# Kernel tuning notes

Hardware: AMD Instinct MI355X
Metric: run time of the kernel (lower is better)

The kernel has to match this reference:

```python
import jax, jax.numpy as jnp
import numpy as np

B, S, D, H = 2, 2048, 1024, 16
HD = D // H  # 64


def setup_inputs() -> dict:
    key = jax.random.key(0)
    ks = jax.random.split(key, 7)
    scale = 1.0 / np.sqrt(D)
    return {
        "embeddings": jax.random.normal(ks[0], (B, S, D), dtype=jnp.float32),
        "W_kv": jax.random.uniform(ks[1], (D, 2 * D), jnp.float32, -scale, scale),
        "b_kv": jax.random.uniform(ks[2], (2 * D,), jnp.float32, -scale, scale),
        "W_q": jax.random.uniform(ks[3], (D, D), jnp.float32, -scale, scale),
        "b_q": jax.random.uniform(ks[4], (D,), jnp.float32, -scale, scale),
        "W_o": jax.random.uniform(ks[5], (D, D), jnp.float32, -scale, scale),
        "b_o": jax.random.uniform(ks[6], (D,), jnp.float32, -scale, scale),
    }


def reference(embeddings, W_kv, b_kv, W_q, b_q, W_o, b_o):
    # kv projection -> [B, S, H, 2*HD] -> [B, H, S, 2*HD]
    kv = (embeddings @ W_kv + b_kv).reshape(B, S, H, 2 * HD).transpose(0, 2, 1, 3)
    q = (embeddings @ W_q + b_q).reshape(B, S, H, HD).transpose(0, 2, 1, 3)
    k, v = kv[..., :HD], kv[..., HD:]
    # naive scaled dot-product attention (full [B,H,S,S] score matrix)
    scores = jnp.einsum("bhqd,bhkd->bhqk", q, k) / jnp.sqrt(jnp.float32(HD))
    attn = jax.nn.softmax(scores, axis=-1)
    ctx = jnp.einsum("bhqk,bhkd->bhqd", attn, v)  # [B,H,S,HD]
    ctx = ctx.transpose(0, 2, 1, 3).reshape(B, S, D)
    return ctx @ W_o + b_o
```

## Files before the change

### kernel.cpp

```cpp
#include <hip/hip_runtime.h>
#include <hip/hip_bf16.h>


typedef unsigned short ushort;
typedef __attribute__((ext_vector_type(4))) float f32x4;
typedef __attribute__((ext_vector_type(16))) float f32x16;
typedef __attribute__((ext_vector_type(8))) __bf16 bf16x8;
typedef __attribute__((ext_vector_type(8))) unsigned short u16x8;
typedef __attribute__((ext_vector_type(4))) unsigned short u16x4;
typedef __attribute__((ext_vector_type(4))) unsigned int u32x4;

#define LOG2E 1.44269504088896340736f

constexpr int Bc = 2, Sc = 2048, Dc = 1024, Hc = 16, HDc = 64;

__device__ inline ushort f2bf(float f) {
    unsigned u = __builtin_bit_cast(unsigned, f);
    u += 0x7fffu + ((u >> 16) & 1u);
    return (ushort)(u >> 16);
}

__device__ inline float fexp2(float x) {
#if __has_builtin(__builtin_amdgcn_exp2f)
    return __builtin_amdgcn_exp2f(x);
#else
    return exp2f(x);
#endif
}

__device__ inline void gload16(const void* g, void* l) {
    __builtin_amdgcn_global_load_lds((const __attribute__((address_space(1))) void*)g,
                                     (__attribute__((address_space(3))) void*)l, 16, 0, 0);
}

__device__ inline f32x4 mfma16(bf16x8 a, bf16x8 b, f32x4 c) {
    return __builtin_amdgcn_mfma_f32_16x16x32_bf16(a, b, c, 0, 0, 0);
}
__device__ inline f32x16 mfma32(bf16x8 a, bf16x8 b, f32x16 c) {
    return __builtin_amdgcn_mfma_f32_32x32x16_bf16(a, b, c, 0, 0, 0);
}
__device__ inline unsigned cvtpk(float lo, float hi_) {
    unsigned r; asm("v_cvt_pk_bf16_f32 %0, %1, %2" : "=v"(r) : "v"(lo), "v"(hi_)); return r;
}
__device__ inline void swap32(unsigned& a, unsigned& b) {
    asm("v_permlane32_swap_b32 %0, %1" : "+v"(a), "+v"(b));
}

__global__ __launch_bounds__(256) void prep_k(const float* __restrict__ emb,
                                              ushort* __restrict__ embb,
                                              const float* __restrict__ Wkv,
                                              const float* __restrict__ Wq,
                                              const float* __restrict__ Wo,
                                              ushort* __restrict__ WtAll) {
    const int bid = blockIdx.x;
    if (bid < 2048) {
        int i = bid * 256 + threadIdx.x;
        const float4* p = (const float4*)emb;
        float4 a = p[2 * i], b = p[2 * i + 1];
        u16x8 r;
        r[0] = f2bf(a.x); r[1] = f2bf(a.y); r[2] = f2bf(a.z); r[3] = f2bf(a.w);
        r[4] = f2bf(b.x); r[5] = f2bf(b.y); r[6] = f2bf(b.z); r[7] = f2bf(b.w);
        ((u16x8*)embb)[i] = r;
        return;
    }
    __shared__ float t[32][33];
    int tb = bid - 2048;
    const float* W; int N, rowofs;
    if (tb < 2048)      { W = Wkv; N = 2048; rowofs = 0; }
    else if (tb < 3072) { W = Wq;  N = 1024; rowofs = 2048; tb -= 2048; }
    else                { W = Wo;  N = 1024; rowofs = 3072; tb -= 3072; }
    const int nbx = N >> 5;
    const int bx = tb % nbx, by = tb / nbx;
    const int tx = threadIdx.x & 31, ty = threadIdx.x >> 5;
    const int bj = bx * 32, bi = by * 32;
#pragma unroll
    for (int i = 0; i < 4; i++) {
        int r = ty + i * 8;
        t[r][tx] = W[(size_t)(bi + r) * N + bj + tx];
    }
    __syncthreads();
#pragma unroll
    for (int i = 0; i < 4; i++) {
        int r = ty + i * 8;
        WtAll[(size_t)(rowofs + bj + r) * 1024 + bi + tx] = f2bf(t[tx][r]);
    }
}

template <int MODE>
__global__ __launch_bounds__(256) void gemm_bt_k(const ushort* __restrict__ A,
                                                 const ushort* __restrict__ Bt,
                                                 const float* __restrict__ bias,
                                                 const float* __restrict__ bias2,
                                                 void* __restrict__ Cout,
                                                 ushort* __restrict__ Vout,
                                                 ushort* __restrict__ Qout,
                                                 int M, int N, int K) {
    __shared__ __align__(16) char sA[2][8192];
    __shared__ __align__(16) char sB[2][8192];
    const int tid = threadIdx.x;
    const int nbc = N >> 7;
    const int cpx = (gridDim.x >> 3);
    const int swzb = (blockIdx.x & 7) * cpx + (blockIdx.x >> 3);
    const int brow = swzb / nbc, bcol = swzb % nbc;
    const int w = tid >> 6, lane = tid & 63;
    const int wr = w >> 1, wc = w & 1;
    const int lg = lane >> 4, l16 = lane & 15;

    f32x4 acc[4][4] = {};

    const int r0 = tid >> 2;
    const int sl = (tid & 3) ^ (r0 & 3);
    const ushort* a0 = A + (size_t)(brow * 128 + r0) * K + sl * 8;
    const ushort* a1 = A + (size_t)(brow * 128 + 64 + r0) * K + sl * 8;
    const ushort* b0 = Bt + (size_t)(bcol * 128 + r0) * K + sl * 8;
    const ushort* b1 = Bt + (size_t)(bcol * 128 + 64 + r0) * K + sl * 8;

    const int arow = wr * 64 + l16;
    const int bcolr = wc * 64 + l16;

    auto STAGE = [&](int buf, int k0) {
        gload16(a0 + k0, sA[buf] + w * 1024);
        gload16(a1 + k0, sA[buf] + 4096 + w * 1024);
        gload16(b0 + k0, sB[buf] + w * 1024);
        gload16(b1 + k0, sB[buf] + 4096 + w * 1024);
    };

    const int nk = K >> 5;
    STAGE(0, 0);

    for (int k0 = 0; k0 < nk; k0++) {
        const int buf = k0 & 1;
        if (k0 < nk - 1) {
            STAGE(buf ^ 1, (k0 + 1) << 5);
            asm volatile("s_waitcnt vmcnt(4)" ::: "memory");
        } else {
            asm volatile("s_waitcnt vmcnt(0)" ::: "memory");
        }
        __builtin_amdgcn_s_barrier();
        __builtin_amdgcn_sched_barrier(0);

        bf16x8 af[4], bfr[4];
#pragma unroll
        for (int rf = 0; rf < 4; rf++) {
            int rr = arow + rf * 16;
            af[rf] = *(const bf16x8*)(sA[buf] + rr * 64 + ((lg * 16) ^ ((rr & 3) << 4)));
        }
#pragma unroll
        for (int cf = 0; cf < 4; cf++) {
            int rr = bcolr + cf * 16;
            bfr[cf] = *(const bf16x8*)(sB[buf] + rr * 64 + ((lg * 16) ^ ((rr & 3) << 4)));
        }
#pragma unroll
        for (int rf = 0; rf < 4; rf++)
#pragma unroll
            for (int cf = 0; cf < 4; cf++)
                acc[rf][cf] = mfma16(af[rf], bfr[cf], acc[rf][cf]);
        __builtin_amdgcn_s_barrier();
    }

#pragma unroll
    for (int cf = 0; cf < 4; cf++) {
        const int col = bcol * 128 + wc * 64 + cf * 16 + l16;
        if constexpr (MODE == 3) {
            if (col < 2048) {
                const float bv = bias[col];
                const int h = col >> 7, lo = col & 127;
#pragma unroll
                for (int rf = 0; rf < 4; rf++) {
                    int row = brow * 128 + wr * 64 + rf * 16 + lg * 4;
                    int b = row >> 11, s = row & 2047;
                    if (lo < 64) {
                        ushort* Kout = (ushort*)Cout;
#pragma unroll
                        for (int r = 0; r < 4; r++)
                            Kout[((size_t)(b * 16 + h) * 2048 + s + r) * 64 + lo] =
                                f2bf(acc[rf][cf][r] + bv);
                    } else {
                        u16x4 pk;
#pragma unroll
                        for (int r = 0; r < 4; r++) pk[r] = f2bf(acc[rf][cf][r] + bv);
                        *(u16x4*)(Vout + ((size_t)(b * 16 + h) * 64 + (lo - 64)) * 2048 + s) = pk;
                    }
                }
            } else {
                const int qc = col - 2048;
                const float bv = bias2[qc];
                const float qs = 0.125f * LOG2E;
#pragma unroll
                for (int rf = 0; rf < 4; rf++) {
                    int row = brow * 128 + wr * 64 + rf * 16 + lg * 4;
#pragma unroll
                    for (int r = 0; r < 4; r++)
                        Qout[(size_t)(row + r) * 1024 + qc] =
                            f2bf((acc[rf][cf][r] + bv) * qs);
                }
            }
        } else {
            const float bv = bias[col];
#pragma unroll
            for (int rf = 0; rf < 4; rf++) {
                int row = brow * 128 + wr * 64 + rf * 16 + lg * 4;
#pragma unroll
                for (int r = 0; r < 4; r++) {
                    float v = acc[rf][cf][r] + bv;
                    if (MODE == 1) ((float*)Cout)[(size_t)(row + r) * N + col] = v;
                    else           ((ushort*)Cout)[(size_t)(row + r) * N + col] = f2bf(v);
                }
            }
        }
    }
}

__global__ __launch_bounds__(256, 2) void attn2_k(const ushort* __restrict__ Qg,
                                                  const ushort* __restrict__ Kg,
                                                  const ushort* __restrict__ Vg,
                                                  ushort* __restrict__ ctx) {
    __shared__ __align__(16) char sK[2][8192];
    __shared__ __align__(16) char sV[2][8192];
    __shared__ float lx2[256];
    const int tid = threadIdx.x;
    const int wg = ((blockIdx.x & 7) << 6) | (blockIdx.x >> 3);
    const int bh = wg >> 4, qt = wg & 15;
    const int b = bh >> 4, h = bh & 15;
    const int w = tid >> 6, lane = tid & 63;
    const int ql = lane & 31, hi = lane >> 5;
    const int ksub = w & 1;
    const int qq = w >> 1;

    const ushort* Kh = Kg + (size_t)bh * (Sc * 64);
    const ushort* Vh = Vg + (size_t)bh * (64 * Sc);

    const int qrow0 = qt * 128 + qq * 64 + ql;
    bf16x8 qf[2][4];
#pragma unroll
    for (int qg = 0; qg < 2; qg++) {
        const ushort* qp = Qg + ((size_t)(b * Sc + qrow0 + qg * 32)) * Dc + h * HDc + hi * 8;
#pragma unroll
        for (int jd = 0; jd < 4; jd++) qf[qg][jd] = *(const bf16x8*)(qp + jd * 16);
    }

    const u16x8 ones_u = {0x3F80, 0x3F80, 0x3F80, 0x3F80, 0x3F80, 0x3F80, 0x3F80, 0x3F80};
    const bf16x8 ones8 = __builtin_bit_cast(bf16x8, ones_u);

    const int rw = w * 16 + (lane >> 3);
    const int sl = (lane & 7) ^ (lane >> 3);

    f32x16 o[2][2] = {};
    f32x16 ls[2] = {};
    const float MH = 8.0f * LOG2E;
    const int sw = (ql & 7) << 4;

    auto STAGE = [&](int buf, int kt) {
#pragma unroll
        for (int j = 0; j < 2; j++) {
            gload16(Kh + (size_t)(kt * 64 + rw + 8 * j) * 64 + sl * 8,
                    sK[buf] + w * 2048 + j * 1024);
            gload16(Vh + (size_t)(rw + 8 * j) * Sc + kt * 64 + sl * 8,
                    sV[buf] + w * 2048 + j * 1024);
        }
    };

    int cur = 0;
    STAGE(0, 0);

    constexpr int NT = Sc / 64;
    for (int kt = 0; kt < NT; kt++) {
        if (kt < NT - 1) {
            STAGE(cur ^ 1, kt + 1);
            asm volatile("s_waitcnt vmcnt(4)" ::: "memory");
        } else {
            asm volatile("s_waitcnt vmcnt(0)" ::: "memory");
        }
        __builtin_amdgcn_s_barrier();
        __builtin_amdgcn_sched_barrier(0);

        bf16x8 kf[4];
        {
            const char* kb = sK[cur] + (ksub * 32 + ql) * 128;
#pragma unroll
            for (int jd = 0; jd < 4; jd++)
                kf[jd] = *(const bf16x8*)(kb + ((jd * 32 + hi * 16) ^ sw));
        }

        f32x16 st[2];
#pragma unroll
        for (int qg = 0; qg < 2; qg++)
#pragma unroll
            for (int i = 0; i < 16; i++) st[qg][i] = -MH;
        __builtin_amdgcn_s_setprio(1);
#pragma unroll
        for (int qg = 0; qg < 2; qg++)
#pragma unroll
            for (int jd = 0; jd < 4; jd++)
                st[qg] = mfma32(kf[jd], qf[qg][jd], st[qg]);
        __builtin_amdgcn_s_setprio(0);

#pragma unroll
        for (int qg = 0; qg < 2; qg++)
#pragma unroll
            for (int i = 0; i < 16; i++) st[qg][i] = fexp2(st[qg][i]);

        bf16x8 pf[2][2];
#pragma unroll
        for (int qg = 0; qg < 2; qg++) {
            unsigned a0 = cvtpk(st[qg][0],  st[qg][1]);
            unsigned a1 = cvtpk(st[qg][2],  st[qg][3]);
            unsigned a2 = cvtpk(st[qg][4],  st[qg][5]);
            unsigned a3 = cvtpk(st[qg][6],  st[qg][7]);
            swap32(a0, a2); swap32(a1, a3);
            u32x4 f0v = {a0, a1, a2, a3};
            pf[qg][0] = __builtin_bit_cast(bf16x8, f0v);
            unsigned c0 = cvtpk(st[qg][8],  st[qg][9]);
            unsigned c1 = cvtpk(st[qg][10], st[qg][11]);
            unsigned c2 = cvtpk(st[qg][12], st[qg][13]);
            unsigned c3 = cvtpk(st[qg][14], st[qg][15]);
            swap32(c0, c2); swap32(c1, c3);
            u32x4 f1v = {c0, c1, c2, c3};
            pf[qg][1] = __builtin_bit_cast(bf16x8, f1v);
        }

        bf16x8 vf[2][2];
#pragma unroll
        for (int dg = 0; dg < 2; dg++) {
            const char* vb = sV[cur] + (dg * 32 + ql) * 128;
#pragma unroll
            for (int ks = 0; ks < 2; ks++)
                vf[dg][ks] = *(const bf16x8*)(vb + ((ksub * 64 + ks * 32 + hi * 16) ^ sw));
        }

        __builtin_amdgcn_s_setprio(1);
#pragma unroll
        for (int qg = 0; qg < 2; qg++)
#pragma unroll
            for (int ks = 0; ks < 2; ks++) {
                o[0][qg] = mfma32(vf[0][ks], pf[qg][ks], o[0][qg]);
                o[1][qg] = mfma32(vf[1][ks], pf[qg][ks], o[1][qg]);
                ls[qg]   = mfma32(ones8,     pf[qg][ks], ls[qg]);
            }
        __builtin_amdgcn_s_setprio(0);

        __builtin_amdgcn_s_barrier();
        cur ^= 1;
    }

    __syncthreads();
    float* ox = qq ? (float*)sV : (float*)sK;
    if (ksub) {
#pragma unroll
        for (int dg = 0; dg < 2; dg++)
#pragma unroll
            for (int qg = 0; qg < 2; qg++)
#pragma unroll
                for (int i = 0; i < 16; i++)
                    ox[((dg * 2 + qg) * 16 + i) * 64 + lane] = o[dg][qg][i];
        lx2[(qq * 2 + 0) * 64 + lane] = ls[0][0];
        lx2[(qq * 2 + 1) * 64 + lane] = ls[1][0];
    }
    __syncthreads();
    if (!ksub) {
#pragma unroll
        for (int dg = 0; dg < 2; dg++)
#pragma unroll
            for (int qg = 0; qg < 2; qg++)
#pragma unroll
                for (int i = 0; i < 16; i++)
                    o[dg][qg][i] += ox[((dg * 2 + qg) * 16 + i) * 64 + lane];
        const float inv0 = 1.0f / (ls[0][0] + lx2[(qq * 2 + 0) * 64 + lane]);
        const float inv1 = 1.0f / (ls[1][0] + lx2[(qq * 2 + 1) * 64 + lane]);
#pragma unroll
        for (int qg = 0; qg < 2; qg++) {
            const float inv = qg ? inv1 : inv0;
            ushort* cp = ctx + ((size_t)(b * Sc + qrow0 + qg * 32)) * Dc + h * HDc;
#pragma unroll
            for (int dg = 0; dg < 2; dg++)
#pragma unroll
                for (int g = 0; g < 4; g++) {
                    u16x4 pk;
#pragma unroll
                    for (int r = 0; r < 4; r++)
                        pk[r] = f2bf(o[dg][qg][g * 4 + r] * inv);
                    *(u16x4*)(cp + dg * 32 + g * 8 + hi * 4) = pk;
                }
        }
    }
}

extern "C" void kernel_launch(void* const* d_in, const int* in_sizes, int n_in,
                              void* d_out, int out_size, void* d_ws, size_t ws_size,
                              hipStream_t stream) {
    const float* emb  = (const float*)d_in[0];
    const float* W_kv = (const float*)d_in[1];
    const float* b_kv = (const float*)d_in[2];
    const float* W_q  = (const float*)d_in[3];
    const float* b_q  = (const float*)d_in[4];
    const float* W_o  = (const float*)d_in[5];
    const float* b_o  = (const float*)d_in[6];
    float* out = (float*)d_out;

    const int BS = Bc * Sc;
    ushort* embb  = (ushort*)d_ws;
    ushort* wallt = embb  + (size_t)BS * Dc;
    ushort* wot   = wallt + (size_t)3 * Dc * Dc;
    ushort* Kb    = wallt + (size_t)4 * Dc * Dc;
    ushort* Vtb   = Kb    + (size_t)32 * Sc * HDc;
    ushort* Qb    = Vtb   + (size_t)32 * Sc * HDc;
    ushort* ctxb  = Qb    + (size_t)BS * Dc;

    prep_k<<<6144, 256, 0, stream>>>(emb, embb, W_kv, W_q, W_o, wallt);

    gemm_bt_k<3><<<(BS / 128) * (3072 / 128), 256, 0, stream>>>(
        embb, wallt, b_kv, b_q, Kb, Vtb, Qb, BS, 3072, Dc);

    attn2_k<<<Bc * Hc * (Sc / 128), 256, 0, stream>>>(Qb, Kb, Vtb, ctxb);

    gemm_bt_k<1><<<(BS / 128) * (Dc / 128), 256, 0, stream>>>(
        ctxb, wot, b_o, nullptr, out, nullptr, nullptr, BS, Dc, Dc);
}
```

Baseline: 115.0 us.

## Use 256x256-tile 512-thread GEMM kernel for fused QKV projection

Replaces the 128x128-tile QKV projection GEMM with a new 256x256-tile kernel using 8 waves and BK=64 double-buffered LDS staging with an XOR swizzle. Each wave computes 128x64, which raises arithmetic intensity per LDS byte and halves global traffic per FLOP. The grid becomes 16x12=192 blocks, fewer than the CU count on MI355X, so some CUs sit idle. The 128 KB of LDS per block may also limit occupancy. The older MODE 3 epilogue is removed from the generic GEMM.

```diff
diff --git a/kernel.cpp b/kernel.cpp
--- a/kernel.cpp
+++ b/kernel.cpp
@@ -86,14 +86,127 @@
     }
 }
 
+__global__ __launch_bounds__(512, 2) void gemm256_kv_k(const ushort* __restrict__ A,
+                                                       const ushort* __restrict__ Bt,
+                                                       const float* __restrict__ bias,
+                                                       const float* __restrict__ bias2,
+                                                       ushort* __restrict__ Kout,
+                                                       ushort* __restrict__ Vout,
+                                                       ushort* __restrict__ Qout,
+                                                       int N, int K) {
+    __shared__ __align__(16) char sA[2][32768];
+    __shared__ __align__(16) char sB[2][32768];
+    const int tid = threadIdx.x;
+    const int nbc = N >> 8;
+    const int cpx = (gridDim.x >> 3);
+    const int swzb = (blockIdx.x & 7) * cpx + (blockIdx.x >> 3);
+    const int brow = swzb / nbc, bcol = swzb % nbc;
+    const int w = tid >> 6, lane = tid & 63;
+    const int wr = w >> 2, wc = w & 3;
+    const int lg = lane >> 4, l16 = lane & 15;
+
+    f32x4 acc[8][4] = {};
+
+    const int srow = tid >> 3;
+    const int schunk = (tid & 7) ^ (srow & 7);
+    const ushort* aP[4];
+    const ushort* bP[4];
+#pragma unroll
+    for (int s = 0; s < 4; s++) {
+        aP[s] = A  + (size_t)(brow * 256 + s * 64 + srow) * K + schunk * 8;
+        bP[s] = Bt + (size_t)(bcol * 256 + s * 64 + srow) * K + schunk * 8;
+    }
+
+    auto STAGE_ALL = [&](int buf, int k0) {
+#pragma unroll
+        for (int s = 0; s < 4; s++)
+            gload16(aP[s] + k0, sA[buf] + s * 8192 + w * 1024);
+#pragma unroll
+        for (int s = 0; s < 4; s++)
+            gload16(bP[s] + k0, sB[buf] + s * 8192 + w * 1024);
+    };
+
+    const int aro = wr * 128 + l16;
+    const int bro = wc * 64 + l16;
+    const int axor = l16 & 7;
+
+    const int nk = K >> 6;
+    STAGE_ALL(0, 0);
+
+    for (int kt = 0; kt < nk; kt++) {
+        const int buf = kt & 1;
+        if (kt < nk - 1) {
+            STAGE_ALL(buf ^ 1, (kt + 1) << 6);
+            asm volatile("s_waitcnt vmcnt(8)" ::: "memory");
+        } else {
+            asm volatile("s_waitcnt vmcnt(0)" ::: "memory");
+        }
+        __builtin_amdgcn_s_barrier();
+        __builtin_amdgcn_sched_barrier(0);
+
+#pragma unroll
+        for (int ks = 0; ks < 2; ks++) {
+            bf16x8 af[8], bfr[4];
+#pragma unroll
+            for (int rf = 0; rf < 8; rf++)
+                af[rf] = *(const bf16x8*)(sA[buf] + (aro + rf * 16) * 128 +
+                                          ((((ks << 2) | lg) ^ axor) << 4));
+#pragma unroll
+            for (int cf = 0; cf < 4; cf++)
+                bfr[cf] = *(const bf16x8*)(sB[buf] + (bro + cf * 16) * 128 +
+                                           ((((ks << 2) | lg) ^ axor) << 4));
+#pragma unroll
+            for (int rf = 0; rf < 8; rf++)
+#pragma unroll
+                for (int cf = 0; cf < 4; cf++)
+                    acc[rf][cf] = mfma16(af[rf], bfr[cf], acc[rf][cf]);
+        }
+        __builtin_amdgcn_s_barrier();
+    }
+
+#pragma unroll
+    for (int cf = 0; cf < 4; cf++) {
+        const int col = bcol * 256 + wc * 64 + cf * 16 + l16;
+        if (col < 2048) {
+            const float bv = bias[col];
+            const int h = col >> 7, lo = col & 127;
+#pragma unroll
+            for (int rf = 0; rf < 8; rf++) {
+                int row = brow * 256 + wr * 128 + rf * 16 + lg * 4;
+                int b = row >> 11, s = row & 2047;
+                if (lo < 64) {
+#pragma unroll
+                    for (int r = 0; r < 4; r++)
+                        Kout[((size_t)(b * 16 + h) * 2048 + s + r) * 64 + lo] =
+                            f2bf(acc[rf][cf][r] + bv);
+                } else {
+                    u16x4 pk;
+#pragma unroll
+                    for (int r = 0; r < 4; r++) pk[r] = f2bf(acc[rf][cf][r] + bv);
+                    *(u16x4*)(Vout + ((size_t)(b * 16 + h) * 64 + (lo - 64)) * 2048 + s) = pk;
+                }
+            }
+        } else {
+            const int qc = col - 2048;
+            const float bv = bias2[qc];
+            const float qs = 0.125f * LOG2E;
+#pragma unroll
+            for (int rf = 0; rf < 8; rf++) {
+                int row = brow * 256 + wr * 128 + rf * 16 + lg * 4;
+#pragma unroll
+                for (int r = 0; r < 4; r++)
+                    Qout[(size_t)(row + r) * 1024 + qc] =
+                        f2bf((acc[rf][cf][r] + bv) * qs);
+            }
+        }
+    }
+}
+
 template <int MODE>
 __global__ __launch_bounds__(256) void gemm_bt_k(const ushort* __restrict__ A,
                                                  const ushort* __restrict__ Bt,
                                                  const float* __restrict__ bias,
-                                                 const float* __restrict__ bias2,
                                                  void* __restrict__ Cout,
-                                                 ushort* __restrict__ Vout,
-                                                 ushort* __restrict__ Qout,
                                                  int M, int N, int K) {
     __shared__ __align__(16) char sA[2][8192];
     __shared__ __align__(16) char sB[2][8192];
@@ -161,51 +274,15 @@
 #pragma unroll
     for (int cf = 0; cf < 4; cf++) {
         const int col = bcol * 128 + wc * 64 + cf * 16 + l16;
-        if constexpr (MODE == 3) {
-            if (col < 2048) {
-                const float bv = bias[col];
-                const int h = col >> 7, lo = col & 127;
-#pragma unroll
-                for (int rf = 0; rf < 4; rf++) {
-                    int row = brow * 128 + wr * 64 + rf * 16 + lg * 4;
-                    int b = row >> 11, s = row & 2047;
-                    if (lo < 64) {
-                        ushort* Kout = (ushort*)Cout;
-#pragma unroll
-                        for (int r = 0; r < 4; r++)
-                            Kout[((size_t)(b * 16 + h) * 2048 + s + r) * 64 + lo] =
-                                f2bf(acc[rf][cf][r] + bv);
-                    } else {
-                        u16x4 pk;
-#pragma unroll
-                        for (int r = 0; r < 4; r++) pk[r] = f2bf(acc[rf][cf][r] + bv);
-                        *(u16x4*)(Vout + ((size_t)(b * 16 + h) * 64 + (lo - 64)) * 2048 + s) = pk;
-                    }
-                }
-            } else {
-                const int qc = col - 2048;
-                const float bv = bias2[qc];
-                const float qs = 0.125f * LOG2E;
-#pragma unroll
-                for (int rf = 0; rf < 4; rf++) {
-                    int row = brow * 128 + wr * 64 + rf * 16 + lg * 4;
-#pragma unroll
-                    for (int r = 0; r < 4; r++)
-                        Qout[(size_t)(row + r) * 1024 + qc] =
-                            f2bf((acc[rf][cf][r] + bv) * qs);
-                }
-            }
-        } else {
-            const float bv = bias[col];
-#pragma unroll
-            for (int rf = 0; rf < 4; rf++) {
-                int row = brow * 128 + wr * 64 + rf * 16 + lg * 4;
-#pragma unroll
-                for (int r = 0; r < 4; r++) {
-                    float v = acc[rf][cf][r] + bv;
-                    if (MODE == 1) ((float*)Cout)[(size_t)(row + r) * N + col] = v;
-                    else           ((ushort*)Cout)[(size_t)(row + r) * N + col] = f2bf(v);
-                }
+        const float bv = bias[col];
+#pragma unroll
+        for (int rf = 0; rf < 4; rf++) {
+            int row = brow * 128 + wr * 64 + rf * 16 + lg * 4;
+#pragma unroll
+            for (int r = 0; r < 4; r++) {
+                float v = acc[rf][cf][r] + bv;
+                if (MODE == 1) ((float*)Cout)[(size_t)(row + r) * N + col] = v;
+                else           ((ushort*)Cout)[(size_t)(row + r) * N + col] = f2bf(v);
             }
         }
     }
@@ -408,11 +485,11 @@
 
     prep_k<<<6144, 256, 0, stream>>>(emb, embb, W_kv, W_q, W_o, wallt);
 
-    gemm_bt_k<3><<<(BS / 128) * (3072 / 128), 256, 0, stream>>>(
-        embb, wallt, b_kv, b_q, Kb, Vtb, Qb, BS, 3072, Dc);
+    gemm256_kv_k<<<(BS / 256) * (3072 / 256), 512, 0, stream>>>(
+        embb, wallt, b_kv, b_q, Kb, Vtb, Qb, 3072, Dc);
 
     attn2_k<<<Bc * Hc * (Sc / 128), 256, 0, stream>>>(Qb, Kb, Vtb, ctxb);
 
     gemm_bt_k<1><<<(BS / 128) * (Dc / 128), 256, 0, stream>>>(
-        ctxb, wot, b_o, nullptr, out, nullptr, nullptr, BS, Dc, Dc);
-}
+        ctxb, wot, b_o, out, BS, Dc, Dc);
+}
```

Result: slower. 118.9 us (+3.4%).
